# Performance work log

Hardware: AMD Instinct MI355X
Metric: run time of the kernel (lower is better)

The kernel has to match this reference:

```python
import jax, jax.numpy as jnp
import numpy as np

B, T, N, C, H = 64, 12, 1370, 8, 64

def setup_inputs() -> dict:
    key = jax.random.key(0)
    ks = jax.random.split(key, 7)
    s_ih = 1.0 / np.sqrt(H)
    inp = {
        "x": jax.random.normal(ks[0], (B, T, N, C), dtype=jnp.float32),
        # PyTorch nn.LSTM params, gate order (i, f, g, o)
        "W_ih": jax.random.uniform(ks[1], (4 * H, C), jnp.float32, -s_ih, s_ih),
        "W_hh": jax.random.uniform(ks[2], (4 * H, H), jnp.float32, -s_ih, s_ih),
        "b_ih": jax.random.uniform(ks[3], (4 * H,), jnp.float32, -s_ih, s_ih),
        "b_hh": jax.random.uniform(ks[4], (4 * H,), jnp.float32, -s_ih, s_ih),
        "W_fc": jax.random.uniform(ks[5], (C, H), jnp.float32, -s_ih, s_ih),
        "b_fc": jax.random.uniform(ks[6], (C,), jnp.float32, -s_ih, s_ih),
    }
    return inp

def reference(x, W_ih, W_hh, b_ih, b_hh, W_fc, b_fc):
    Bx, Tx, Nx, Cx = x.shape
    Hh = W_hh.shape[1]
    # (B, T, N, C) -> (B*N, T, C): shared-weight LSTM over all node sequences
    xr = jnp.transpose(x, (0, 2, 1, 3)).reshape(Bx * Nx, Tx, Cx)
    # Precompute input projections for all timesteps: (B*N, T, 4H)
    x_gates = jnp.einsum('btc,gc->btg', xr, W_ih) + b_ih
    # time-major for scan: (T, B*N, 4H)
    x_gates = jnp.moveaxis(x_gates, 1, 0)

    def step(carry, xg):
        h, c = carry
        gates = xg + h @ W_hh.T + b_hh  # (B*N, 4H)
        i, f, g, o = jnp.split(gates, 4, axis=-1)
        i = jax.nn.sigmoid(i)
        f = jax.nn.sigmoid(f)
        g = jnp.tanh(g)
        o = jax.nn.sigmoid(o)
        c = f * c + i * g
        h = o * jnp.tanh(c)
        return (h, c), None

    h0 = jnp.zeros((Bx * Nx, Hh), dtype=x.dtype)
    c0 = jnp.zeros((Bx * Nx, Hh), dtype=x.dtype)
    (h_last, _), _ = jax.lax.scan(step, (h0, c0), x_gates)

    y_flat = h_last @ W_fc.T + b_fc  # (B*N, C)
    return y_flat.reshape(Bx, Nx, Cx)
```

## Files before the change

### kernel.cpp

```cpp
#include <hip/hip_runtime.h>

#define T_ 12
#define N_ 1370
#define MSEQ 32
#define LDA 72
#define LDX 20
#define NBLK 2740

typedef __attribute__((ext_vector_type(8))) short short8;
typedef __attribute__((ext_vector_type(4))) float floatx4;

#define NLOG2E -1.4426950408889634f
#define TLOG2E 2.8853900817779268f

__device__ __forceinline__ short f2bf(float x) {
  unsigned u = __builtin_bit_cast(unsigned, x);
  u = (u + 0x7fffu + ((u >> 16) & 1u)) >> 16;
  return (short)u;
}
__device__ __forceinline__ unsigned pk_bf16(float a, float b) {
  unsigned r;
  asm("v_cvt_pk_bf16_f32 %0, %1, %2" : "=v"(r) : "v"(a), "v"(b));
  return r;
}
__device__ __forceinline__ short8 load_w8s(const float* __restrict__ p, float s) {
  short8 r;
#pragma unroll
  for (int j = 0; j < 8; ++j) r[j] = f2bf(p[j] * s);
  return r;
}

__global__ void __launch_bounds__(256, 4) lstm_kernel(
    const float* __restrict__ x, const float* __restrict__ W_ih,
    const float* __restrict__ W_hh, const float* __restrict__ b_ih,
    const float* __restrict__ b_hh, const float* __restrict__ W_fc,
    const float* __restrict__ b_fc, float* __restrict__ out) {
  __shared__ short hbuf[2][MSEQ][LDA];
  __shared__ short xls[T_][MSEQ][LDX];

  const int tid = threadIdx.x;
  const int wave = tid >> 6;
  const int lane = tid & 63;
  const int m16 = lane & 15;
  const int q = lane >> 4;
  const int blk = blockIdx.x;

  const int urow = wave * 16 + m16;
  short8 wA[4][3];
#pragma unroll
  for (int g = 0; g < 4; ++g) {
    const float sg = (g == 2) ? TLOG2E : NLOG2E;
    const int grow = g * 64 + urow;
    const float* wr = W_hh + grow * 64;
    wA[g][0] = load_w8s(wr + q * 8, sg);
    wA[g][1] = load_w8s(wr + 32 + q * 8, sg);
    short8 z = {0, 0, 0, 0, 0, 0, 0, 0};
    if (q == 0) {
      wA[g][2] = load_w8s(W_ih + grow * 8, sg);
    } else if (q == 1) {
      z[0] = f2bf(sg * (b_ih[grow] + b_hh[grow]));
      wA[g][2] = z;
    } else {
      wA[g][2] = z;
    }
  }

  {
    int* hp = (int*)hbuf;
#pragma unroll
    for (int i = tid; i < (2 * MSEQ * LDA) / 2; i += 256) hp[i] = 0;
    int* xp = (int*)xls;
#pragma unroll
    for (int i = tid; i < (T_ * MSEQ * LDX) / 2; i += 256) xp[i] = 0;
  }
  __syncthreads();

  {
    const int xseq = tid >> 3, xc = tid & 7;
    const int s0 = blk * MSEQ + xseq;
    const int bidx = s0 / N_;
    const int nidx = s0 - bidx * N_;
    const float* xp = x + ((size_t)(bidx * T_) * N_ + nidx) * 8 + xc;
#pragma unroll
    for (int t = 0; t < T_; ++t) {
      xls[t][xseq][xc] = f2bf(xp[(size_t)t * (N_ * 8)]);
      if (xc == 0) xls[t][xseq][8] = (short)0x3F80;
    }
  }
  __syncthreads();

  const int xoff = q ? 8 : 0;
  const floatx4 zacc = {0.0f, 0.0f, 0.0f, 0.0f};

  float cst[2][4];
#pragma unroll
  for (int nt = 0; nt < 2; ++nt)
#pragma unroll
    for (int r = 0; r < 4; ++r) cst[nt][r] = 0.0f;

  for (int t = 0; t < T_; ++t) {
    const int rb = t & 1, wb = rb ^ 1;
#pragma unroll
    for (int nt = 0; nt < 2; ++nt) {
      const int srow = nt * 16 + m16;
      short8 b0 = *(const short8*)&hbuf[rb][srow][q * 8];
      short8 b1 = *(const short8*)&hbuf[rb][srow][32 + q * 8];
      short8 bx = *(const short8*)&xls[t][srow][xoff];
      floatx4 gi = __builtin_amdgcn_mfma_f32_16x16x32_bf16(wA[0][0], b0, zacc, 0, 0, 0);
      floatx4 gf = __builtin_amdgcn_mfma_f32_16x16x32_bf16(wA[1][0], b0, zacc, 0, 0, 0);
      floatx4 gg = __builtin_amdgcn_mfma_f32_16x16x32_bf16(wA[2][0], b0, zacc, 0, 0, 0);
      floatx4 go = __builtin_amdgcn_mfma_f32_16x16x32_bf16(wA[3][0], b0, zacc, 0, 0, 0);
      gi = __builtin_amdgcn_mfma_f32_16x16x32_bf16(wA[0][1], b1, gi, 0, 0, 0);
      gf = __builtin_amdgcn_mfma_f32_16x16x32_bf16(wA[1][1], b1, gf, 0, 0, 0);
      gg = __builtin_amdgcn_mfma_f32_16x16x32_bf16(wA[2][1], b1, gg, 0, 0, 0);
      go = __builtin_amdgcn_mfma_f32_16x16x32_bf16(wA[3][1], b1, go, 0, 0, 0);
      gi = __builtin_amdgcn_mfma_f32_16x16x32_bf16(wA[0][2], bx, gi, 0, 0, 0);
      gf = __builtin_amdgcn_mfma_f32_16x16x32_bf16(wA[1][2], bx, gf, 0, 0, 0);
      gg = __builtin_amdgcn_mfma_f32_16x16x32_bf16(wA[2][2], bx, gg, 0, 0, 0);
      go = __builtin_amdgcn_mfma_f32_16x16x32_bf16(wA[3][2], bx, go, 0, 0, 0);
      float hv[4];
#pragma unroll
      for (int r = 0; r < 4; ++r) {
        float di = 1.0f + __builtin_amdgcn_exp2f(gi[r]);
        float df = 1.0f + __builtin_amdgcn_exp2f(gf[r]);
        float dg = 1.0f + __builtin_amdgcn_exp2f(gg[r]);
        float dq = 1.0f + __builtin_amdgcn_exp2f(go[r]);
        float pa = di * df, pb = dg * dq;
        float rp = __builtin_amdgcn_rcpf(pa * pb);
        float iv = rp * df * pb;
        float fv = rp * di * pb;
        float gv = fmaf(-2.0f, rp * pa * dq, 1.0f);
        float ov = rp * pa * dg;
        float cc = fmaf(fv, cst[nt][r], iv * gv);
        cst[nt][r] = cc;
        float dt = 1.0f + __builtin_amdgcn_exp2f(cc * TLOG2E);
        float tc = fmaf(-2.0f, __builtin_amdgcn_rcpf(dt), 1.0f);
        hv[r] = ov * tc;
      }
      unsigned long long pk =
          (unsigned long long)pk_bf16(hv[0], hv[1]) |
          ((unsigned long long)pk_bf16(hv[2], hv[3]) << 32);
      *(unsigned long long*)&hbuf[wb][srow][wave * 16 + q * 4] = pk;
    }
    __syncthreads();
  }

  if (wave < 2) {
    short8 f0, f1;
    short8 z = {0, 0, 0, 0, 0, 0, 0, 0};
    if (m16 < 8) {
      const float* wr = W_fc + m16 * 64;
      f0 = load_w8s(wr + q * 8, 1.0f);
      f1 = load_w8s(wr + 32 + q * 8, 1.0f);
    } else {
      f0 = z;
      f1 = z;
    }
    const int srow = wave * 16 + m16;
    short8 h0 = *(const short8*)&hbuf[0][srow][q * 8];
    short8 h1 = *(const short8*)&hbuf[0][srow][32 + q * 8];
    floatx4 acc = __builtin_amdgcn_mfma_f32_16x16x32_bf16(f0, h0, zacc, 0, 0, 0);
    acc = __builtin_amdgcn_mfma_f32_16x16x32_bf16(f1, h1, acc, 0, 0, 0);
    if (q < 2) {
      const int orow = blk * MSEQ + srow;
#pragma unroll
      for (int r = 0; r < 4; ++r)
        out[orow * 8 + q * 4 + r] = acc[r] + b_fc[q * 4 + r];
    }
  }
}

extern "C" void kernel_launch(void* const* d_in, const int* in_sizes, int n_in,
                              void* d_out, int out_size, void* d_ws,
                              size_t ws_size, hipStream_t stream) {
  const float* x    = (const float*)d_in[0];
  const float* W_ih = (const float*)d_in[1];
  const float* W_hh = (const float*)d_in[2];
  const float* b_ih = (const float*)d_in[3];
  const float* b_hh = (const float*)d_in[4];
  const float* W_fc = (const float*)d_in[5];
  const float* b_fc = (const float*)d_in[6];
  float* out = (float*)d_out;
  hipLaunchKernelGGL(lstm_kernel, dim3(NBLK), dim3(256), 0, stream,
                     x, W_ih, W_hh, b_ih, b_hh, W_fc, b_fc, out);
}
```

Baseline: 169.9 us.

## Keep x in registers and stream per-step input into the h buffer

Replaces the per-block shared-memory x tile covering all timesteps with per-thread bf16-packed registers loaded up front. Each step writes the next timestep's x slice into the h double buffer, which is widened to hold the x columns and the bias-one column. This shrinks LDS use so launch bounds can target 5 blocks per CU instead of 4, and the time loop is fully unrolled. The cost is extra VGPR pressure from the packed x values and the unrolled loop, plus an extra LDS write inside every step.

```diff
diff --git a/kernel.cpp b/kernel.cpp
--- a/kernel.cpp
+++ b/kernel.cpp
@@ -3,8 +3,8 @@
 #define T_ 12
 #define N_ 1370
 #define MSEQ 32
-#define LDA 72
-#define LDX 20
+#define LDA 88
+#define HBUF (MSEQ * LDA)
 #define NBLK 2740
 
 typedef __attribute__((ext_vector_type(8))) short short8;
@@ -30,13 +30,12 @@
   return r;
 }
 
-__global__ void __launch_bounds__(256, 4) lstm_kernel(
+__global__ void __launch_bounds__(256, 5) lstm_kernel(
     const float* __restrict__ x, const float* __restrict__ W_ih,
     const float* __restrict__ W_hh, const float* __restrict__ b_ih,
     const float* __restrict__ b_hh, const float* __restrict__ W_fc,
     const float* __restrict__ b_fc, float* __restrict__ out) {
-  __shared__ short hbuf[2][MSEQ][LDA];
-  __shared__ short xls[T_][MSEQ][LDX];
+  __shared__ short hbuf[2 * HBUF + 8];
 
   const int tid = threadIdx.x;
   const int wave = tid >> 6;
@@ -44,6 +43,20 @@
   const int m16 = lane & 15;
   const int q = lane >> 4;
   const int blk = blockIdx.x;
+
+  const int xseq = tid >> 3, xc = tid & 7;
+  unsigned xpk[6];
+  {
+    const int s0 = blk * MSEQ + xseq;
+    const int bidx = s0 / N_;
+    const int nidx = s0 - bidx * N_;
+    const float* xp = x + ((size_t)(bidx * T_) * N_ + nidx) * 8 + xc;
+    float xv[T_];
+#pragma unroll
+    for (int t = 0; t < T_; ++t) xv[t] = xp[(size_t)t * (N_ * 8)];
+#pragma unroll
+    for (int i = 0; i < 6; ++i) xpk[i] = pk_bf16(xv[2 * i], xv[2 * i + 1]);
+  }
 
   const int urow = wave * 16 + m16;
   short8 wA[4][3];
@@ -68,44 +81,36 @@
   {
     int* hp = (int*)hbuf;
 #pragma unroll
-    for (int i = tid; i < (2 * MSEQ * LDA) / 2; i += 256) hp[i] = 0;
-    int* xp = (int*)xls;
-#pragma unroll
-    for (int i = tid; i < (T_ * MSEQ * LDX) / 2; i += 256) xp[i] = 0;
+    for (int i = tid; i < (2 * HBUF + 8) / 2; i += 256) hp[i] = 0;
   }
   __syncthreads();
-
-  {
-    const int xseq = tid >> 3, xc = tid & 7;
-    const int s0 = blk * MSEQ + xseq;
-    const int bidx = s0 / N_;
-    const int nidx = s0 - bidx * N_;
-    const float* xp = x + ((size_t)(bidx * T_) * N_ + nidx) * 8 + xc;
-#pragma unroll
-    for (int t = 0; t < T_; ++t) {
-      xls[t][xseq][xc] = f2bf(xp[(size_t)t * (N_ * 8)]);
-      if (xc == 0) xls[t][xseq][8] = (short)0x3F80;
-    }
-  }
+  if (tid < 2 * MSEQ)
+    hbuf[(tid >> 5) * HBUF + (tid & 31) * LDA + 72] = (short)0x3F80;
+  hbuf[xseq * LDA + 64 + xc] = (short)xpk[0];
   __syncthreads();
 
-  const int xoff = q ? 8 : 0;
   const floatx4 zacc = {0.0f, 0.0f, 0.0f, 0.0f};
-
   float cst[2][4];
 #pragma unroll
   for (int nt = 0; nt < 2; ++nt)
 #pragma unroll
     for (int r = 0; r < 4; ++r) cst[nt][r] = 0.0f;
 
+#pragma unroll
   for (int t = 0; t < T_; ++t) {
     const int rb = t & 1, wb = rb ^ 1;
+    if (t + 1 < T_) {
+      unsigned p = xpk[(t + 1) >> 1];
+      short xv = (short)(((t + 1) & 1) ? (p >> 16) : p);
+      hbuf[wb * HBUF + xseq * LDA + 64 + xc] = xv;
+    }
 #pragma unroll
     for (int nt = 0; nt < 2; ++nt) {
       const int srow = nt * 16 + m16;
-      short8 b0 = *(const short8*)&hbuf[rb][srow][q * 8];
-      short8 b1 = *(const short8*)&hbuf[rb][srow][32 + q * 8];
-      short8 bx = *(const short8*)&xls[t][srow][xoff];
+      const short* base = &hbuf[rb * HBUF + srow * LDA];
+      short8 b0 = *(const short8*)(base + q * 8);
+      short8 b1 = *(const short8*)(base + 32 + q * 8);
+      short8 b2 = *(const short8*)(base + 64 + q * 8);
       floatx4 gi = __builtin_amdgcn_mfma_f32_16x16x32_bf16(wA[0][0], b0, zacc, 0, 0, 0);
       floatx4 gf = __builtin_amdgcn_mfma_f32_16x16x32_bf16(wA[1][0], b0, zacc, 0, 0, 0);
       floatx4 gg = __builtin_amdgcn_mfma_f32_16x16x32_bf16(wA[2][0], b0, zacc, 0, 0, 0);
@@ -114,10 +119,10 @@
       gf = __builtin_amdgcn_mfma_f32_16x16x32_bf16(wA[1][1], b1, gf, 0, 0, 0);
       gg = __builtin_amdgcn_mfma_f32_16x16x32_bf16(wA[2][1], b1, gg, 0, 0, 0);
       go = __builtin_amdgcn_mfma_f32_16x16x32_bf16(wA[3][1], b1, go, 0, 0, 0);
-      gi = __builtin_amdgcn_mfma_f32_16x16x32_bf16(wA[0][2], bx, gi, 0, 0, 0);
-      gf = __builtin_amdgcn_mfma_f32_16x16x32_bf16(wA[1][2], bx, gf, 0, 0, 0);
-      gg = __builtin_amdgcn_mfma_f32_16x16x32_bf16(wA[2][2], bx, gg, 0, 0, 0);
-      go = __builtin_amdgcn_mfma_f32_16x16x32_bf16(wA[3][2], bx, go, 0, 0, 0);
+      gi = __builtin_amdgcn_mfma_f32_16x16x32_bf16(wA[0][2], b2, gi, 0, 0, 0);
+      gf = __builtin_amdgcn_mfma_f32_16x16x32_bf16(wA[1][2], b2, gf, 0, 0, 0);
+      gg = __builtin_amdgcn_mfma_f32_16x16x32_bf16(wA[2][2], b2, gg, 0, 0, 0);
+      go = __builtin_amdgcn_mfma_f32_16x16x32_bf16(wA[3][2], b2, go, 0, 0, 0);
       float hv[4];
 #pragma unroll
       for (int r = 0; r < 4; ++r) {
@@ -129,8 +134,9 @@
         float rp = __builtin_amdgcn_rcpf(pa * pb);
         float iv = rp * df * pb;
         float fv = rp * di * pb;
-        float gv = fmaf(-2.0f, rp * pa * dq, 1.0f);
-        float ov = rp * pa * dg;
+        float t1 = rp * pa;
+        float gv = fmaf(-2.0f, t1 * dq, 1.0f);
+        float ov = t1 * dg;
         float cc = fmaf(fv, cst[nt][r], iv * gv);
         cst[nt][r] = cc;
         float dt = 1.0f + __builtin_amdgcn_exp2f(cc * TLOG2E);
@@ -140,7 +146,7 @@
       unsigned long long pk =
           (unsigned long long)pk_bf16(hv[0], hv[1]) |
           ((unsigned long long)pk_bf16(hv[2], hv[3]) << 32);
-      *(unsigned long long*)&hbuf[wb][srow][wave * 16 + q * 4] = pk;
+      *(unsigned long long*)&hbuf[wb * HBUF + srow * LDA + wave * 16 + q * 4] = pk;
     }
     __syncthreads();
   }
@@ -157,8 +163,8 @@
       f1 = z;
     }
     const int srow = wave * 16 + m16;
-    short8 h0 = *(const short8*)&hbuf[0][srow][q * 8];
-    short8 h1 = *(const short8*)&hbuf[0][srow][32 + q * 8];
+    short8 h0 = *(const short8*)&hbuf[srow * LDA + q * 8];
+    short8 h1 = *(const short8*)&hbuf[srow * LDA + 32 + q * 8];
     floatx4 acc = __builtin_amdgcn_mfma_f32_16x16x32_bf16(f0, h0, zacc, 0, 0, 0);
     acc = __builtin_amdgcn_mfma_f32_16x16x32_bf16(f1, h1, acc, 0, 0, 0);
     if (q < 2) {
```

New measurement: 189.1 us. +11.3%, slower.
